# Kernel optimization log

Hardware: AMD Instinct MI355X
Metric: run time of the kernel (lower is better)

## Reference

```python
import jax, jax.numpy as jnp
import numpy as np

VOCAB_SIZE = 119547  # bert-base-multilingual-cased
B, S, H = 64, 512, 768


def setup_inputs() -> dict:
    key = jax.random.key(0)
    k1, k2, k3, k4 = jax.random.split(key, 4)
    hidden_states = jax.random.normal(k1, (B, S, H), dtype=jnp.float32)
    input_ids = jax.random.randint(k2, (B, S), 0, VOCAB_SIZE, dtype=jnp.int64)
    attention_mask = jnp.ones((B, S), dtype=jnp.int32)
    W1 = jax.random.normal(k3, (H, H), dtype=jnp.float32) * (1.0 / np.sqrt(H))
    b1 = jnp.zeros((H,), dtype=jnp.float32)
    W2 = jax.random.normal(k4, (H, 1), dtype=jnp.float32) * (1.0 / np.sqrt(H))
    b2 = jnp.zeros((1,), dtype=jnp.float32)
    return {"hidden_states": hidden_states, "input_ids": input_ids,
            "attention_mask": attention_mask, "W1": W1, "b1": b1, "W2": W2, "b2": b2}


def reference(hidden_states, input_ids, attention_mask, W1, b1, W2, b2):
    # token_importance MLP (dropout = identity at eval): [B,S,H] -> [B,S]
    h = jax.nn.relu(jnp.einsum('bsh,hk->bsk', hidden_states, W1) + b1)
    importance = (jnp.einsum('bsh,ho->bso', h, W2) + b2)[..., 0]  # [B,S]
    token_weights = jnp.log1p(jax.nn.relu(importance)) * attention_mask.astype(jnp.float32)
    # scatter-max into vocab-sized sparse doc vector.
    # Masked positions have weight 0; buffer init 0 and weights >= 0, so
    # scattering 0 is equivalent to skipping them (matches the torch loop).
    batch_idx = jnp.arange(hidden_states.shape[0])[:, None]  # [B,1]
    sparse_repr = jnp.zeros((hidden_states.shape[0], VOCAB_SIZE), dtype=token_weights.dtype)
    sparse_repr = sparse_repr.at[batch_idx, input_ids].max(token_weights)
    return sparse_repr, token_weights
```

## Files before the change

### kernel.cpp

```cpp
#include <hip/hip_runtime.h>
#include <math.h>
#include <stdint.h>

#define VOCAB 119547
#define NB    64
#define NS    512
#define NH    768
#define M_TOT (NB * NS)

typedef _Float16 half8_t __attribute__((ext_vector_type(8)));
typedef _Float16 half4_t __attribute__((ext_vector_type(4)));
typedef float f32x4 __attribute__((ext_vector_type(4)));

__device__ __forceinline__ void gload_lds16(const void* g, void* l) {
    __builtin_amdgcn_global_load_lds(
        (const __attribute__((address_space(1))) uint32_t*)g,
        (__attribute__((address_space(3))) uint32_t*)l, 16, 0, 0);
}

__global__ void prep(const float* __restrict__ X, const float* __restrict__ W1,
                     float4* __restrict__ sparse4, float* __restrict__ imp4_,
                     _Float16* __restrict__ Xh, _Float16* __restrict__ W1T) {
    long i = (long)blockIdx.x * blockDim.x + threadIdx.x;
    long stride = (long)gridDim.x * blockDim.x;
    const float4 z = make_float4(0.f, 0.f, 0.f, 0.f);
    const long nsp4 = (long)NB * VOCAB / 4;
    for (long j = i; j < nsp4; j += stride) sparse4[j] = z;
    float4* imp4 = (float4*)imp4_;
    for (long j = i; j < M_TOT / 4; j += stride) imp4[j] = z;
    const long nx4 = (long)M_TOT * NH / 4;
    const float4* X4 = (const float4*)X;
    half4_t* Xh4 = (half4_t*)Xh;
    for (long j = i; j < nx4; j += stride) {
        float4 v = X4[j];
        half4_t h;
        h[0] = (_Float16)v.x; h[1] = (_Float16)v.y;
        h[2] = (_Float16)v.z; h[3] = (_Float16)v.w;
        Xh4[j] = h;
    }
    const long nw4 = (long)NH * NH / 4;
    half4_t* W1T4 = (half4_t*)W1T;
    for (long j = i; j < nw4; j += stride) {
        int n  = (int)(j / (NH / 4));
        int k4 = (int)(j % (NH / 4)) * 4;
        half4_t h;
#pragma unroll
        for (int q = 0; q < 4; ++q) h[q] = (_Float16)W1[(long)(k4 + q) * NH + n];
        W1T4[j] = h;
    }
}

__global__ __launch_bounds__(256) void gemm_f16(
    const _Float16* __restrict__ Xh,
    const _Float16* __restrict__ W1T,
    const float* __restrict__ b1,
    const float* __restrict__ W2v,
    float* __restrict__ imp)
{
    __shared__ __align__(16) _Float16 As[128 * 32];
    __shared__ __align__(16) _Float16 Bs[128 * 32];

    const int tid  = threadIdx.x;
    const int lane = tid & 63;
    const int wid  = tid >> 6;
    const int wm   = wid >> 1;
    const int wn   = wid & 1;

    const int bid = blockIdx.x;
    const int wg  = (bid & 7) * 192 + (bid >> 3);
    const int nt  = wg % 6;
    const int mt  = wg / 6;
    const int m0  = mt * 128;
    const int n0  = nt * 128;

    const int c0 = tid, c1 = tid + 256;
    const int r0 = c0 >> 2, r1 = c1 >> 2;
    const int sk0 = ((c0 & 3) ^ ((r0 >> 1) & 3)) * 8;
    const int sk1 = ((c1 & 3) ^ ((r1 >> 1) & 3)) * 8;
    const _Float16* gA0 = Xh  + (long)(m0 + r0) * NH + sk0;
    const _Float16* gA1 = Xh  + (long)(m0 + r1) * NH + sk1;
    const _Float16* gB0 = W1T + (long)(n0 + r0) * NH + sk0;
    const _Float16* gB1 = W1T + (long)(n0 + r1) * NH + sk1;
    _Float16* lA0 = As + c0 * 8;  _Float16* lA1 = As + c1 * 8;
    _Float16* lB0 = Bs + c0 * 8;  _Float16* lB1 = Bs + c1 * 8;

    const int lr = lane & 15;
    const int ls = lane >> 4;
    const int s2 = ls ^ ((lr >> 1) & 3);
    int offA[4], offB[4];
#pragma unroll
    for (int f = 0; f < 4; ++f) {
        offA[f] = (wm * 64 + f * 16 + lr) * 32 + s2 * 8;
        offB[f] = (wn * 64 + f * 16 + lr) * 32 + s2 * 8;
    }

    f32x4 acc[4][4];
#pragma unroll
    for (int a = 0; a < 4; ++a)
#pragma unroll
        for (int b = 0; b < 4; ++b) acc[a][b] = (f32x4){0.f, 0.f, 0.f, 0.f};

#pragma unroll 1
    for (int kk = 0; kk < NH / 32; ++kk) {
        gload_lds16(gA0, lA0);
        gload_lds16(gA1, lA1);
        gload_lds16(gB0, lB0);
        gload_lds16(gB1, lB1);
        gA0 += 32; gA1 += 32; gB0 += 32; gB1 += 32;
        __syncthreads();

        half8_t af[4], bf[4];
#pragma unroll
        for (int f = 0; f < 4; ++f) af[f] = *(const half8_t*)(As + offA[f]);
#pragma unroll
        for (int f = 0; f < 4; ++f) bf[f] = *(const half8_t*)(Bs + offB[f]);
#pragma unroll
        for (int a = 0; a < 4; ++a)
#pragma unroll
            for (int b = 0; b < 4; ++b)
                acc[a][b] = __builtin_amdgcn_mfma_f32_16x16x32_f16(
                    af[a], bf[b], acc[a][b], 0, 0, 0);
        __syncthreads();
    }

    float b1v[4], w2v[4];
#pragma unroll
    for (int f = 0; f < 4; ++f) {
        int col = n0 + wn * 64 + f * 16 + lr;
        b1v[f] = b1[col];
        w2v[f] = W2v[col];
    }
#pragma unroll
    for (int a = 0; a < 4; ++a)
#pragma unroll
        for (int reg = 0; reg < 4; ++reg) {
            float p = 0.f;
#pragma unroll
            for (int f = 0; f < 4; ++f) {
                float h = fmaxf(acc[a][f][reg] + b1v[f], 0.f);
                p = fmaf(h, w2v[f], p);
            }
            p += __shfl_xor(p, 1);
            p += __shfl_xor(p, 2);
            p += __shfl_xor(p, 4);
            p += __shfl_xor(p, 8);
            if (lr == 0) {
                int row = m0 + wm * 64 + a * 16 + ls * 4 + reg;
                atomicAdd(&imp[row], p);
            }
        }
}

__global__ void finalize(const float* __restrict__ imp,
                         const float* __restrict__ b2,
                         const int* __restrict__ mask,
                         const int* __restrict__ ids,
                         float* __restrict__ tw_out,
                         float* __restrict__ sparse) {
    int i = blockIdx.x * blockDim.x + threadIdx.x;
    if (i >= M_TOT) return;
    float v = fmaxf(imp[i] + b2[0], 0.f);
    float tw = log1pf(v) * (float)mask[i];
    tw_out[i] = tw;
    int b  = i >> 9;
    int id = ids[i];
    unsigned int* addr = (unsigned int*)&sparse[(long)b * VOCAB + id];
    atomicMax(addr, __float_as_uint(tw));
}

__global__ void zero_regions(float4* __restrict__ a, long na4,
                             float4* __restrict__ b, long nb4) {
    long i = (long)blockIdx.x * blockDim.x + threadIdx.x;
    long stride = (long)gridDim.x * blockDim.x;
    const float4 z = make_float4(0.f, 0.f, 0.f, 0.f);
    for (long j = i; j < na4; j += stride) a[j] = z;
    for (long j = i; j < nb4; j += stride) b[j] = z;
}

__global__ __launch_bounds__(256) void gemm_importance(
    const float* __restrict__ X, const float* __restrict__ W1,
    const float* __restrict__ b1, const float* __restrict__ W2v,
    float* __restrict__ imp)
{
    __shared__ float As_[16][64];
    __shared__ float Bs_[16][128];
    const int tid = threadIdx.x;
    const int m0 = blockIdx.x * 64, n0 = blockIdx.y * 128;
    const int tx = tid & 31, ty = tid >> 5;
    float acc[8][4];
#pragma unroll
    for (int r = 0; r < 8; ++r)
#pragma unroll
        for (int c = 0; c < 4; ++c) acc[r][c] = 0.f;
    const int arow = tid >> 2, ac = (tid & 3) * 4;
    const float* Xp = X + (long)(m0 + arow) * NH + ac;
    for (int k0 = 0; k0 < NH; k0 += 16) {
        float4 av = *(const float4*)(Xp + k0);
        As_[ac + 0][arow] = av.x; As_[ac + 1][arow] = av.y;
        As_[ac + 2][arow] = av.z; As_[ac + 3][arow] = av.w;
        int f = tid, br = f >> 5, bc = (f & 31) * 4;
        *(float4*)&Bs_[br][bc] = *(const float4*)&W1[(long)(k0 + br) * NH + n0 + bc];
        f = tid + 256; br = f >> 5; bc = (f & 31) * 4;
        *(float4*)&Bs_[br][bc] = *(const float4*)&W1[(long)(k0 + br) * NH + n0 + bc];
        __syncthreads();
#pragma unroll
        for (int k = 0; k < 16; ++k) {
            float4 a0 = *(const float4*)&As_[k][ty * 8];
            float4 a1 = *(const float4*)&As_[k][ty * 8 + 4];
            float4 bv = *(const float4*)&Bs_[k][tx * 4];
            float a[8] = {a0.x, a0.y, a0.z, a0.w, a1.x, a1.y, a1.z, a1.w};
            float bb[4] = {bv.x, bv.y, bv.z, bv.w};
#pragma unroll
            for (int r = 0; r < 8; ++r)
#pragma unroll
                for (int c = 0; c < 4; ++c)
                    acc[r][c] = fmaf(a[r], bb[c], acc[r][c]);
        }
        __syncthreads();
    }
    float b1v[4], w2v[4];
#pragma unroll
    for (int c = 0; c < 4; ++c) {
        int col = n0 + tx * 4 + c;
        b1v[c] = b1[col]; w2v[c] = W2v[col];
    }
#pragma unroll
    for (int r = 0; r < 8; ++r) {
        float p = 0.f;
#pragma unroll
        for (int c = 0; c < 4; ++c)
            p = fmaf(fmaxf(acc[r][c] + b1v[c], 0.f), w2v[c], p);
#pragma unroll
        for (int mdel = 16; mdel >= 1; mdel >>= 1) p += __shfl_xor(p, mdel);
        if (tx == 0) atomicAdd(&imp[m0 + ty * 8 + r], p);
    }
}

extern "C" void kernel_launch(void* const* d_in, const int* in_sizes, int n_in,
                              void* d_out, int out_size, void* d_ws, size_t ws_size,
                              hipStream_t stream) {
    const float* X    = (const float*)d_in[0];
    const int*   ids  = (const int*)d_in[1];
    const int*   mask = (const int*)d_in[2];
    const float* W1   = (const float*)d_in[3];
    const float* b1   = (const float*)d_in[4];
    const float* W2   = (const float*)d_in[5];
    const float* b2   = (const float*)d_in[6];

    float* sparse = (float*)d_out;
    float* tw_out = sparse + (long)NB * VOCAB;
    float* imp    = (float*)d_ws;

    const size_t impB = (size_t)M_TOT * 4;
    const size_t XhB  = (size_t)M_TOT * NH * 2;
    const size_t W1TB = (size_t)NH * NH * 2;
    const size_t need = impB + XhB + W1TB;

    if (ws_size >= need) {
        _Float16* Xh  = (_Float16*)((char*)d_ws + impB);
        _Float16* W1T = (_Float16*)((char*)d_ws + impB + XhB);
        prep<<<2048, 256, 0, stream>>>(X, W1, (float4*)sparse, imp, Xh, W1T);
        gemm_f16<<<(M_TOT / 128) * (NH / 128), 256, 0, stream>>>(
            Xh, W1T, b1, W2, imp);
        finalize<<<M_TOT / 256, 256, 0, stream>>>(imp, b2, mask, ids, tw_out, sparse);
    } else {
        zero_regions<<<2048, 256, 0, stream>>>(
            (float4*)sparse, (long)NB * VOCAB / 4, (float4*)imp, M_TOT / 4);
        dim3 grid(M_TOT / 64, NH / 128);
        gemm_importance<<<grid, 256, 0, stream>>>(X, W1, b1, W2, imp);
        finalize<<<M_TOT / 256, 256, 0, stream>>>(imp, b2, mask, ids, tw_out, sparse);
    }
}
```

Measured before the change: 244.5 us.

## Fuse fp32-to-fp16 conversion of X into GEMM with double-buffered LDS pipeline

The separate prep pass that converted the whole hidden_states tensor to fp16 is removed. The GEMM now loads fp32 X directly into registers, converts it, and writes it into swizzled LDS. LDS is double-buffered so the next tile's global loads overlap the MFMA compute on the current tile, with one barrier per step instead of two. This removes a full read of X plus a write and re-read of the fp16 copy, at the cost of twice as many fp32 bytes of A read per GEMM tile (X is re-read across the six N tiles), more registers, and doubled LDS.

```diff
diff --git a/kernel.cpp b/kernel.cpp
--- a/kernel.cpp
+++ b/kernel.cpp
@@ -18,26 +18,16 @@
         (__attribute__((address_space(3))) uint32_t*)l, 16, 0, 0);
 }
 
-__global__ void prep(const float* __restrict__ X, const float* __restrict__ W1,
-                     float4* __restrict__ sparse4, float* __restrict__ imp4_,
-                     _Float16* __restrict__ Xh, _Float16* __restrict__ W1T) {
+__global__ void prep(const float* __restrict__ W1,
+                     float4* __restrict__ sparse4, float* __restrict__ imp_,
+                     _Float16* __restrict__ W1T) {
     long i = (long)blockIdx.x * blockDim.x + threadIdx.x;
     long stride = (long)gridDim.x * blockDim.x;
     const float4 z = make_float4(0.f, 0.f, 0.f, 0.f);
     const long nsp4 = (long)NB * VOCAB / 4;
     for (long j = i; j < nsp4; j += stride) sparse4[j] = z;
-    float4* imp4 = (float4*)imp4_;
+    float4* imp4 = (float4*)imp_;
     for (long j = i; j < M_TOT / 4; j += stride) imp4[j] = z;
-    const long nx4 = (long)M_TOT * NH / 4;
-    const float4* X4 = (const float4*)X;
-    half4_t* Xh4 = (half4_t*)Xh;
-    for (long j = i; j < nx4; j += stride) {
-        float4 v = X4[j];
-        half4_t h;
-        h[0] = (_Float16)v.x; h[1] = (_Float16)v.y;
-        h[2] = (_Float16)v.z; h[3] = (_Float16)v.w;
-        Xh4[j] = h;
-    }
     const long nw4 = (long)NH * NH / 4;
     half4_t* W1T4 = (half4_t*)W1T;
     for (long j = i; j < nw4; j += stride) {
@@ -50,15 +40,15 @@
     }
 }
 
-__global__ __launch_bounds__(256) void gemm_f16(
-    const _Float16* __restrict__ Xh,
+__global__ __launch_bounds__(256, 4) void gemm_f16(
+    const float* __restrict__ X,
     const _Float16* __restrict__ W1T,
     const float* __restrict__ b1,
     const float* __restrict__ W2v,
     float* __restrict__ imp)
 {
-    __shared__ __align__(16) _Float16 As[128 * 32];
-    __shared__ __align__(16) _Float16 Bs[128 * 32];
+    __shared__ __align__(16) _Float16 As[2][128 * 32];
+    __shared__ __align__(16) _Float16 Bs[2][128 * 32];
 
     const int tid  = threadIdx.x;
     const int lane = tid & 63;
@@ -77,12 +67,13 @@
     const int r0 = c0 >> 2, r1 = c1 >> 2;
     const int sk0 = ((c0 & 3) ^ ((r0 >> 1) & 3)) * 8;
     const int sk1 = ((c1 & 3) ^ ((r1 >> 1) & 3)) * 8;
-    const _Float16* gA0 = Xh  + (long)(m0 + r0) * NH + sk0;
-    const _Float16* gA1 = Xh  + (long)(m0 + r1) * NH + sk1;
     const _Float16* gB0 = W1T + (long)(n0 + r0) * NH + sk0;
     const _Float16* gB1 = W1T + (long)(n0 + r1) * NH + sk1;
-    _Float16* lA0 = As + c0 * 8;  _Float16* lA1 = As + c1 * 8;
-    _Float16* lB0 = Bs + c0 * 8;  _Float16* lB1 = Bs + c1 * 8;
+
+    const int ar = tid >> 3;
+    const int kc = tid & 7;
+    const float* gA = X + (long)(m0 + ar) * NH + kc * 4;
+    const int aw = ((kc >> 1) ^ ((ar >> 1) & 3)) * 8 + (kc & 1) * 4;
 
     const int lr = lane & 15;
     const int ls = lane >> 4;
@@ -100,28 +91,62 @@
 #pragma unroll
         for (int b = 0; b < 4; ++b) acc[a][b] = (f32x4){0.f, 0.f, 0.f, 0.f};
 
+    float4 Areg[4];
+
+#define LOADA(T)                                                            \
+    _Pragma("unroll") for (int i = 0; i < 4; ++i)                           \
+        Areg[i] = *(const float4*)(gA + (T) * 32 + (long)i * 32 * NH);
+
+#define CVTWRITE(BUF)                                                       \
+    _Pragma("unroll") for (int i = 0; i < 4; ++i) {                         \
+        half4_t h;                                                          \
+        h[0] = (_Float16)Areg[i].x; h[1] = (_Float16)Areg[i].y;             \
+        h[2] = (_Float16)Areg[i].z; h[3] = (_Float16)Areg[i].w;             \
+        *(half4_t*)(As[BUF] + (ar + 32 * i) * 32 + aw) = h;                 \
+    }
+
+#define STAGEB(T, BUF)                                                      \
+    gload_lds16(gB0 + (T) * 32, Bs[BUF] + c0 * 8);                          \
+    gload_lds16(gB1 + (T) * 32, Bs[BUF] + c1 * 8);
+
+#define COMPUTE(BUF)                                                        \
+    {                                                                       \
+        half8_t af[4], bf[4];                                               \
+        _Pragma("unroll") for (int f = 0; f < 4; ++f)                       \
+            af[f] = *(const half8_t*)(As[BUF] + offA[f]);                   \
+        _Pragma("unroll") for (int f = 0; f < 4; ++f)                       \
+            bf[f] = *(const half8_t*)(Bs[BUF] + offB[f]);                   \
+        _Pragma("unroll") for (int a = 0; a < 4; ++a)                       \
+            _Pragma("unroll") for (int b = 0; b < 4; ++b)                   \
+                acc[a][b] = __builtin_amdgcn_mfma_f32_16x16x32_f16(         \
+                    af[a], bf[b], acc[a][b], 0, 0, 0);                      \
+    }
+
+#define KSTEP(T, CUR, NXT)                                                  \
+    LOADA((T) + 1);                                                         \
+    STAGEB((T) + 1, NXT);                                                   \
+    COMPUTE(CUR);                                                           \
+    CVTWRITE(NXT);                                                          \
+    __syncthreads();
+
+    LOADA(0);
+    STAGEB(0, 0);
+    CVTWRITE(0);
+    __syncthreads();
+
 #pragma unroll 1
-    for (int kk = 0; kk < NH / 32; ++kk) {
-        gload_lds16(gA0, lA0);
-        gload_lds16(gA1, lA1);
-        gload_lds16(gB0, lB0);
-        gload_lds16(gB1, lB1);
-        gA0 += 32; gA1 += 32; gB0 += 32; gB1 += 32;
-        __syncthreads();
-
-        half8_t af[4], bf[4];
-#pragma unroll
-        for (int f = 0; f < 4; ++f) af[f] = *(const half8_t*)(As + offA[f]);
-#pragma unroll
-        for (int f = 0; f < 4; ++f) bf[f] = *(const half8_t*)(Bs + offB[f]);
-#pragma unroll
-        for (int a = 0; a < 4; ++a)
-#pragma unroll
-            for (int b = 0; b < 4; ++b)
-                acc[a][b] = __builtin_amdgcn_mfma_f32_16x16x32_f16(
-                    af[a], bf[b], acc[a][b], 0, 0, 0);
-        __syncthreads();
-    }
+    for (int t = 0; t < 22; t += 2) {
+        KSTEP(t, 0, 1);
+        KSTEP(t + 1, 1, 0);
+    }
+    KSTEP(22, 0, 1);
+    COMPUTE(1);
+
+#undef LOADA
+#undef CVTWRITE
+#undef STAGEB
+#undef COMPUTE
+#undef KSTEP
 
     float b1v[4], w2v[4];
 #pragma unroll
@@ -252,16 +277,14 @@
     float* imp    = (float*)d_ws;
 
     const size_t impB = (size_t)M_TOT * 4;
-    const size_t XhB  = (size_t)M_TOT * NH * 2;
     const size_t W1TB = (size_t)NH * NH * 2;
-    const size_t need = impB + XhB + W1TB;
+    const size_t need = impB + W1TB;
 
     if (ws_size >= need) {
-        _Float16* Xh  = (_Float16*)((char*)d_ws + impB);
-        _Float16* W1T = (_Float16*)((char*)d_ws + impB + XhB);
-        prep<<<2048, 256, 0, stream>>>(X, W1, (float4*)sparse, imp, Xh, W1T);
+        _Float16* W1T = (_Float16*)((char*)d_ws + impB);
+        prep<<<1024, 256, 0, stream>>>(W1, (float4*)sparse, imp, W1T);
         gemm_f16<<<(M_TOT / 128) * (NH / 128), 256, 0, stream>>>(
-            Xh, W1T, b1, W2, imp);
+            X, W1T, b1, W2, imp);
         finalize<<<M_TOT / 256, 256, 0, stream>>>(imp, b2, mask, ids, tw_out, sparse);
     } else {
         zero_regions<<<2048, 256, 0, stream>>>(
```

Result: no change. 249.1 us (+1.9%).
